# Performance work log

Hardware: AMD Instinct MI355X
Metric: run time of the kernel (lower is better)

## Reference

```python
import jax, jax.numpy as jnp
import numpy as np

NUM_HEADS = 16


def setup_inputs() -> dict:
    key = jax.random.key(0)
    ks = jax.random.split(key, 5)
    B, S, H = 2, 2048, 1024
    scale = 0.02
    return {
        "x": jax.random.normal(ks[0], (B, S, H), dtype=jnp.float32),
        "w_qkv": jax.random.normal(ks[1], (H, 3 * H), dtype=jnp.float32) * scale,
        "b_qkv": jax.random.normal(ks[2], (3 * H,), dtype=jnp.float32) * scale,
        "w_out": jax.random.normal(ks[3], (H, H), dtype=jnp.float32) * scale,
        "b_out": jax.random.normal(ks[4], (H,), dtype=jnp.float32) * scale,
    }


def reference(x, w_qkv, b_qkv, w_out, b_out):
    B, S, H = x.shape
    nh = NUM_HEADS
    hd = H // nh
    attn_scale = 1.0 / np.sqrt(hd).astype(np.float32)

    qkv = x @ w_qkv + b_qkv                       # (B, S, 3H)
    q, k, v = jnp.split(qkv, 3, axis=-1)
    # (B, S, H) -> (B, nh, S, hd)
    to_heads = lambda t: t.reshape(B, S, nh, hd).transpose(0, 2, 1, 3)
    q, k, v = to_heads(q), to_heads(k), to_heads(v)

    scores = jnp.einsum("bhid,bhjd->bhij", q, k) * attn_scale  # (B, nh, S, S)
    # Source masks where triu(ones)==0 -> strictly-lower triangle masked;
    # allowed positions are j >= i (attends to present and future).
    i = jnp.arange(S)[:, None]
    j = jnp.arange(S)[None, :]
    scores = jnp.where(j >= i, scores, -jnp.inf)
    attn = jax.nn.softmax(scores, axis=-1)        # dropout is identity (eval)

    out = jnp.einsum("bhij,bhjd->bhid", attn, v)  # (B, nh, S, hd)
    out = out.transpose(0, 2, 1, 3).reshape(B, S, H)
    return out @ w_out + b_out
```

## Files before the change

kernel.cpp:

```cpp
#include <hip/hip_runtime.h>
#include <hip/hip_bf16.h>
#include <stdint.h>
#include <stddef.h>

typedef __bf16 bf16_t;
typedef __bf16 bf16x4 __attribute__((ext_vector_type(4)));
typedef __bf16 bf16x8 __attribute__((ext_vector_type(8)));
typedef float f32x4 __attribute__((ext_vector_type(4)));

#define MFMA16(a, b, c) __builtin_amdgcn_mfma_f32_16x16x32_bf16(a, b, c, 0, 0, 0)

#define GLL16(g, l)                                                      \
    __builtin_amdgcn_global_load_lds(                                    \
        (const __attribute__((address_space(1))) void*)(g),              \
        (__attribute__((address_space(3))) void*)(l), 16, 0, 0)

#define SEQ 2048
#define NHEAD 16
#define HD 64
#define HID 1024
#define QKV_LD 3072
#define VT_LD 2080

__global__ void cast_f32_bf16(const float* __restrict__ in,
                              bf16_t* __restrict__ out, int n) {
    int i = (blockIdx.x * 256 + threadIdx.x) * 4;
    if (i < n) {
        float4 v = *(const float4*)(in + i);
        bf16x4 o = {(bf16_t)v.x, (bf16_t)v.y, (bf16_t)v.z, (bf16_t)v.w};
        *(bf16x4*)(out + i) = o;
    }
}

__global__ void transpose_cast(const float* __restrict__ W,
                               bf16_t* __restrict__ Wt, int K, int N) {
    __shared__ bf16_t tile[32][33];
    int n0 = blockIdx.x * 32, k0 = blockIdx.y * 32;
    int tx = threadIdx.x, ty = threadIdx.y;
#pragma unroll
    for (int i = 0; i < 4; i++)
        tile[ty + i * 8][tx] = (bf16_t)W[(size_t)(k0 + ty + i * 8) * N + n0 + tx];
    __syncthreads();
#pragma unroll
    for (int i = 0; i < 4; i++)
        Wt[(size_t)(n0 + ty + i * 8) * K + k0 + tx] = tile[tx][ty + i * 8];
}

__global__ __launch_bounds__(256)
void vt_transpose(const bf16_t* __restrict__ qkv, bf16_t* __restrict__ Vt) {
    int s0 = blockIdx.x * 64;
    int bh = blockIdx.y;
    int b = bh >> 4, h = bh & 15;
    int tid = threadIdx.x;
    __shared__ __align__(16) bf16_t tile[64][72];

    int row = tid >> 3, c8 = (tid & 7) * 8;
#pragma unroll
    for (int it = 0; it < 2; it++) {
        int sr = row + it * 32;
        bf16x8 v = *(const bf16x8*)(qkv + ((size_t)b * SEQ + s0 + sr) * QKV_LD +
                                    2 * HID + h * HD + c8);
        *(bf16x8*)(&tile[sr][c8]) = v;
    }
    __syncthreads();
#pragma unroll
    for (int it = 0; it < 2; it++) {
        int d = row + it * 32;
        bf16x8 w;
#pragma unroll
        for (int e = 0; e < 8; e++) w[e] = tile[c8 + e][d];
        *(bf16x8*)(Vt + ((size_t)bh * HD + d) * VT_LD + s0 + c8) = w;
    }
}

template <typename OutT>
__global__ __launch_bounds__(256)
void gemm_bt_bias(const bf16_t* __restrict__ A, const bf16_t* __restrict__ Bt,
                  const float* __restrict__ bias, OutT* __restrict__ C,
                  int M, int N, int K) {
    __shared__ __align__(16) bf16_t As[128][32];
    __shared__ __align__(16) bf16_t Bs[128][32];

    int m0 = blockIdx.y * 128;
    int n0 = blockIdx.x * 128;
    int tid = threadIdx.x;
    int wave = tid >> 6, lane = tid & 63;
    int quad = lane >> 4, l16 = lane & 15;
    int wm = (wave >> 1) * 64, wn = (wave & 1) * 64;

    f32x4 acc[4][4] = {};

    const bf16_t* a_base = A + (size_t)(m0 + wave * 32 + (lane >> 2)) * K + (lane & 3) * 8;
    const bf16_t* b_base = Bt + (size_t)(n0 + wave * 32 + (lane >> 2)) * K + (lane & 3) * 8;
    bf16_t* as_base = &As[wave * 32][0];
    bf16_t* bs_base = &Bs[wave * 32][0];

    for (int k0 = 0; k0 < K; k0 += 32) {
        GLL16(a_base + k0, as_base);
        GLL16(a_base + 16 * K + k0, as_base + 16 * 32);
        GLL16(b_base + k0, bs_base);
        GLL16(b_base + 16 * K + k0, bs_base + 16 * 32);
        __syncthreads();

        bf16x8 af[4], bfr[4];
#pragma unroll
        for (int t = 0; t < 4; t++)
            af[t] = *(const bf16x8*)(&As[wm + t * 16 + l16][quad * 8]);
#pragma unroll
        for (int t = 0; t < 4; t++)
            bfr[t] = *(const bf16x8*)(&Bs[wn + t * 16 + l16][quad * 8]);
#pragma unroll
        for (int mt = 0; mt < 4; mt++)
#pragma unroll
            for (int nt = 0; nt < 4; nt++)
                acc[mt][nt] = MFMA16(af[mt], bfr[nt], acc[mt][nt]);
        __syncthreads();
    }

#pragma unroll
    for (int mt = 0; mt < 4; mt++) {
        int row = m0 + wm + mt * 16 + quad * 4;
#pragma unroll
        for (int nt = 0; nt < 4; nt++) {
            int col = n0 + wn + nt * 16 + l16;
            float bv = bias[col];
#pragma unroll
            for (int r = 0; r < 4; r++)
                C[(size_t)(row + r) * N + col] = (OutT)(acc[mt][nt][r] + bv);
        }
    }
}

__global__ __launch_bounds__(256)
void attn_kernel(const bf16_t* __restrict__ qkv, const bf16_t* __restrict__ Vt,
                 bf16_t* __restrict__ attn_out) {
    int L = blockIdx.y * 16 + blockIdx.x;
    int xcd = L & 7, idx = L >> 3;
    int bh = xcd + 8 * (idx >> 4);
    int xb = idx & 15;
    int b = bh >> 4, h = bh & 15;

    int tid = threadIdx.x, wave = tid >> 6, lane = tid & 63;
    int quad = lane >> 4, l16 = lane & 15;

    const bf16_t* q_g = qkv + (size_t)b * SEQ * QKV_LD + (size_t)h * HD;
    const bf16_t* k_g = q_g + HID;
    const bf16_t* vt_g = Vt + (size_t)bh * HD * VT_LD;

    __shared__ __align__(16) bf16_t Ks[128][72];
    __shared__ __align__(16) bf16_t Vs[64][136];
    __shared__ __align__(16) bf16_t Ps[4][16][136];

    bf16x8 ones;
#pragma unroll
    for (int e = 0; e < 8; e++) ones[e] = (bf16_t)1.0f;

    int krow = tid >> 3, kc8 = (tid & 7) * 8;
    int vrow = tid >> 4, vc8 = (tid & 15) * 8;

#pragma unroll
    for (int phase = 0; phase < 2; phase++) {
        int tile = phase ? (31 - xb) : xb;
        int i0 = tile * 64;
        int iw = i0 + wave * 16;

        bf16x8 qa0 = *(const bf16x8*)(q_g + (size_t)(iw + l16) * QKV_LD + quad * 8);
        bf16x8 qa1 = *(const bf16x8*)(q_g + (size_t)(iw + l16) * QKV_LD + 32 + quad * 8);

        f32x4 o[4] = {};
        f32x4 lacc = {};

        for (int j0 = i0 & ~127; j0 < SEQ; j0 += 128) {
            __syncthreads();
#pragma unroll
            for (int t = 0; t < 4; t++) {
                bf16x8 kv = *(const bf16x8*)(k_g + (size_t)(j0 + krow + t * 32) * QKV_LD + kc8);
                *(bf16x8*)(&Ks[krow + t * 32][kc8]) = kv;
            }
#pragma unroll
            for (int t = 0; t < 4; t++) {
                bf16x8 vv = *(const bf16x8*)(vt_g + (size_t)(vrow + t * 16) * VT_LD + j0 + vc8);
                *(bf16x8*)(&Vs[vrow + t * 16][vc8]) = vv;
            }
            __syncthreads();

            f32x4 s[8];
#pragma unroll
            for (int jt = 0; jt < 8; jt++) {
                bf16x8 kb0 = *(const bf16x8*)(&Ks[jt * 16 + l16][quad * 8]);
                bf16x8 kb1 = *(const bf16x8*)(&Ks[jt * 16 + l16][32 + quad * 8]);
                f32x4 a = {};
                a = MFMA16(qa0, kb0, a);
                a = MFMA16(qa1, kb1, a);
                s[jt] = a;
            }

#pragma unroll
            for (int jt = 0; jt < 8; jt++) {
                int gj = j0 + jt * 16 + l16;
#pragma unroll
                for (int r = 0; r < 4; r++) {
                    int gi = iw + quad * 4 + r;
                    float p = (gj >= gi) ? __expf(s[jt][r] * 0.125f) : 0.0f;
                    Ps[wave][quad * 4 + r][jt * 16 + l16] = (bf16_t)p;
                }
            }

            bf16x8 pa[4];
#pragma unroll
            for (int kk = 0; kk < 4; kk++) {
                pa[kk] = *(const bf16x8*)(&Ps[wave][l16][kk * 32 + quad * 8]);
                lacc = MFMA16(pa[kk], ones, lacc);
            }

#pragma unroll
            for (int nt = 0; nt < 4; nt++) {
#pragma unroll
                for (int kk = 0; kk < 4; kk++) {
                    bf16x8 vb = *(const bf16x8*)(&Vs[nt * 16 + l16][kk * 32 + quad * 8]);
                    o[nt] = MFMA16(pa[kk], vb, o[nt]);
                }
            }
        }

#pragma unroll
        for (int r = 0; r < 4; r++) {
            int gi = iw + quad * 4 + r;
            float inv = 1.0f / lacc[r];
#pragma unroll
            for (int nt = 0; nt < 4; nt++)
                attn_out[(size_t)(b * SEQ + gi) * HID + h * HD + nt * 16 + l16] =
                    (bf16_t)(o[nt][r] * inv);
        }
    }
}

extern "C" void kernel_launch(void* const* d_in, const int* in_sizes, int n_in,
                              void* d_out, int out_size, void* d_ws, size_t ws_size,
                              hipStream_t stream) {
    const float* x     = (const float*)d_in[0];
    const float* w_qkv = (const float*)d_in[1];
    const float* b_qkv = (const float*)d_in[2];
    const float* w_out = (const float*)d_in[3];
    const float* b_out = (const float*)d_in[4];
    float* out = (float*)d_out;

    char* ws = (char*)d_ws;
    bf16_t* xbf   = (bf16_t*)(ws);
    bf16_t* Vt    = (bf16_t*)(ws);
    bf16_t* wqkvT = (bf16_t*)(ws + 8388608);
    bf16_t* woutT = (bf16_t*)(ws + 14680064);
    bf16_t* qkv   = (bf16_t*)(ws + 16777216);
    bf16_t* attn  = (bf16_t*)(ws + 41943040);

    cast_f32_bf16<<<4096, 256, 0, stream>>>(x, xbf, 4096 * 1024);

    transpose_cast<<<dim3(3072 / 32, 1024 / 32), dim3(32, 8), 0, stream>>>(
        w_qkv, wqkvT, 1024, 3072);
    transpose_cast<<<dim3(1024 / 32, 1024 / 32), dim3(32, 8), 0, stream>>>(
        w_out, woutT, 1024, 1024);

    gemm_bt_bias<bf16_t><<<dim3(3072 / 128, 4096 / 128), 256, 0, stream>>>(
        xbf, wqkvT, b_qkv, qkv, 4096, 3072, 1024);

    vt_transpose<<<dim3(SEQ / 64, 2 * NHEAD), 256, 0, stream>>>(qkv, Vt);

    attn_kernel<<<dim3(16, 2 * NHEAD), 256, 0, stream>>>(qkv, Vt, attn);

    gemm_bt_bias<float><<<dim3(1024 / 128, 4096 / 128), 256, 0, stream>>>(
        attn, woutT, b_out, out, 4096, 1024, 1024);
}
```

Before: 205.9 us.

## Fuse prep kernels, split attention tiles per block, narrow output GEMM tiles

Merges the x cast and both weight transpose-casts into one launch. The attention kernel now gives each block a single query tile instead of a paired short/long tile, which doubles the grid. It also reuses the K shared buffer for the P scratch (adding a barrier) and folds the softmax scale and log2e into Q so exp2 can be used. The causal mask is evaluated only on the first key block. The output projection GEMM uses 64-wide N tiles to put more blocks on the device, and attention gets a launch_bounds occupancy hint. The risks are load imbalance from unequal tile lengths, an extra barrier in each loop iteration, and extra bf16 rounding of the pre-scaled Q.

```diff
diff --git a/kernel.cpp b/kernel.cpp
--- a/kernel.cpp
+++ b/kernel.cpp
@@ -22,21 +22,33 @@
 #define QKV_LD 3072
 #define VT_LD 2080
 
-__global__ void cast_f32_bf16(const float* __restrict__ in,
-                              bf16_t* __restrict__ out, int n) {
-    int i = (blockIdx.x * 256 + threadIdx.x) * 4;
-    if (i < n) {
-        float4 v = *(const float4*)(in + i);
+__global__ __launch_bounds__(256)
+void prep_kernel(const float* __restrict__ x, const float* __restrict__ w_qkv,
+                 const float* __restrict__ w_out, bf16_t* __restrict__ xbf,
+                 bf16_t* __restrict__ wqkvT, bf16_t* __restrict__ woutT) {
+    int L = blockIdx.x;
+    int tid = threadIdx.x;
+    if (L < 4096) {
+        int i = (L * 256 + tid) * 4;
+        float4 v = *(const float4*)(x + i);
         bf16x4 o = {(bf16_t)v.x, (bf16_t)v.y, (bf16_t)v.z, (bf16_t)v.w};
-        *(bf16x4*)(out + i) = o;
-    }
-}
-
-__global__ void transpose_cast(const float* __restrict__ W,
-                               bf16_t* __restrict__ Wt, int K, int N) {
+        *(bf16x4*)(xbf + i) = o;
+        return;
+    }
     __shared__ bf16_t tile[32][33];
-    int n0 = blockIdx.x * 32, k0 = blockIdx.y * 32;
-    int tx = threadIdx.x, ty = threadIdx.y;
+    const float* W;
+    bf16_t* Wt;
+    int N, bx, by;
+    if (L < 7168) {
+        int r = L - 4096;
+        W = w_qkv; Wt = wqkvT; N = 3072; bx = r % 96; by = r / 96;
+    } else {
+        int r = L - 7168;
+        W = w_out; Wt = woutT; N = 1024; bx = r % 32; by = r / 32;
+    }
+    int K = 1024;
+    int n0 = bx * 32, k0 = by * 32;
+    int tx = tid & 31, ty = tid >> 5;
 #pragma unroll
     for (int i = 0; i < 4; i++)
         tile[ty + i * 8][tx] = (bf16_t)W[(size_t)(k0 + ty + i * 8) * N + n0 + tx];
@@ -73,46 +85,49 @@
     }
 }
 
-template <typename OutT>
+template <typename OutT, int TN>
 __global__ __launch_bounds__(256)
 void gemm_bt_bias(const bf16_t* __restrict__ A, const bf16_t* __restrict__ Bt,
                   const float* __restrict__ bias, OutT* __restrict__ C,
                   int M, int N, int K) {
+    constexpr int NT = TN / 32;
     __shared__ __align__(16) bf16_t As[128][32];
-    __shared__ __align__(16) bf16_t Bs[128][32];
+    __shared__ __align__(16) bf16_t Bs[TN][32];
 
     int m0 = blockIdx.y * 128;
-    int n0 = blockIdx.x * 128;
+    int n0 = blockIdx.x * TN;
     int tid = threadIdx.x;
     int wave = tid >> 6, lane = tid & 63;
     int quad = lane >> 4, l16 = lane & 15;
-    int wm = (wave >> 1) * 64, wn = (wave & 1) * 64;
-
-    f32x4 acc[4][4] = {};
-
-    const bf16_t* a_base = A + (size_t)(m0 + wave * 32 + (lane >> 2)) * K + (lane & 3) * 8;
-    const bf16_t* b_base = Bt + (size_t)(n0 + wave * 32 + (lane >> 2)) * K + (lane & 3) * 8;
+    int wm = (wave >> 1) * 64, wn = (wave & 1) * (TN / 2);
+
+    f32x4 acc[4][NT] = {};
+
+    const bf16_t* a_base =
+        A + (size_t)(m0 + wave * 32 + (lane >> 2)) * K + (lane & 3) * 8;
+    const bf16_t* b_base =
+        Bt + (size_t)(n0 + wave * (TN / 4) + (lane >> 2)) * K + (lane & 3) * 8;
     bf16_t* as_base = &As[wave * 32][0];
-    bf16_t* bs_base = &Bs[wave * 32][0];
+    bf16_t* bs_base = &Bs[wave * (TN / 4)][0];
 
     for (int k0 = 0; k0 < K; k0 += 32) {
         GLL16(a_base + k0, as_base);
         GLL16(a_base + 16 * K + k0, as_base + 16 * 32);
         GLL16(b_base + k0, bs_base);
-        GLL16(b_base + 16 * K + k0, bs_base + 16 * 32);
-        __syncthreads();
-
-        bf16x8 af[4], bfr[4];
+        if (TN == 128) GLL16(b_base + 16 * K + k0, bs_base + 16 * 32);
+        __syncthreads();
+
+        bf16x8 af[4], bfr[NT];
 #pragma unroll
         for (int t = 0; t < 4; t++)
             af[t] = *(const bf16x8*)(&As[wm + t * 16 + l16][quad * 8]);
 #pragma unroll
-        for (int t = 0; t < 4; t++)
+        for (int t = 0; t < NT; t++)
             bfr[t] = *(const bf16x8*)(&Bs[wn + t * 16 + l16][quad * 8]);
 #pragma unroll
         for (int mt = 0; mt < 4; mt++)
 #pragma unroll
-            for (int nt = 0; nt < 4; nt++)
+            for (int nt = 0; nt < NT; nt++)
                 acc[mt][nt] = MFMA16(af[mt], bfr[nt], acc[mt][nt]);
         __syncthreads();
     }
@@ -121,7 +136,7 @@
     for (int mt = 0; mt < 4; mt++) {
         int row = m0 + wm + mt * 16 + quad * 4;
 #pragma unroll
-        for (int nt = 0; nt < 4; nt++) {
+        for (int nt = 0; nt < NT; nt++) {
             int col = n0 + wn + nt * 16 + l16;
             float bv = bias[col];
 #pragma unroll
@@ -131,13 +146,13 @@
     }
 }
 
-__global__ __launch_bounds__(256)
+__global__ __launch_bounds__(256, 4)
 void attn_kernel(const bf16_t* __restrict__ qkv, const bf16_t* __restrict__ Vt,
                  bf16_t* __restrict__ attn_out) {
-    int L = blockIdx.y * 16 + blockIdx.x;
-    int xcd = L & 7, idx = L >> 3;
-    int bh = xcd + 8 * (idx >> 4);
-    int xb = idx & 15;
+    int L = blockIdx.y * 32 + blockIdx.x;
+    int xcd = L & 7, s5 = L >> 3;
+    int bh = xcd + 8 * (s5 >> 5);
+    int tile = s5 & 31;
     int b = bh >> 4, h = bh & 15;
 
     int tid = threadIdx.x, wave = tid >> 6, lane = tid & 63;
@@ -149,89 +164,106 @@
 
     __shared__ __align__(16) bf16_t Ks[128][72];
     __shared__ __align__(16) bf16_t Vs[64][136];
-    __shared__ __align__(16) bf16_t Ps[4][16][136];
+    bf16_t* Ps_w = &Ks[wave * 32][0];
 
     bf16x8 ones;
 #pragma unroll
     for (int e = 0; e < 8; e++) ones[e] = (bf16_t)1.0f;
+
+    int i0 = tile * 64;
+    int iw = i0 + wave * 16;
+
+    const float QS = 0.125f * 1.44269504088896f;
+    bf16x8 qa0, qa1;
+    {
+        bf16x8 t0 = *(const bf16x8*)(q_g + (size_t)(iw + l16) * QKV_LD + quad * 8);
+        bf16x8 t1 = *(const bf16x8*)(q_g + (size_t)(iw + l16) * QKV_LD + 32 + quad * 8);
+#pragma unroll
+        for (int e = 0; e < 8; e++) {
+            qa0[e] = (bf16_t)((float)t0[e] * QS);
+            qa1[e] = (bf16_t)((float)t1[e] * QS);
+        }
+    }
+
+    f32x4 o[4] = {};
+    f32x4 lacc = {};
 
     int krow = tid >> 3, kc8 = (tid & 7) * 8;
     int vrow = tid >> 4, vc8 = (tid & 15) * 8;
 
-#pragma unroll
-    for (int phase = 0; phase < 2; phase++) {
-        int tile = phase ? (31 - xb) : xb;
-        int i0 = tile * 64;
-        int iw = i0 + wave * 16;
-
-        bf16x8 qa0 = *(const bf16x8*)(q_g + (size_t)(iw + l16) * QKV_LD + quad * 8);
-        bf16x8 qa1 = *(const bf16x8*)(q_g + (size_t)(iw + l16) * QKV_LD + 32 + quad * 8);
-
-        f32x4 o[4] = {};
-        f32x4 lacc = {};
-
-        for (int j0 = i0 & ~127; j0 < SEQ; j0 += 128) {
-            __syncthreads();
-#pragma unroll
-            for (int t = 0; t < 4; t++) {
-                bf16x8 kv = *(const bf16x8*)(k_g + (size_t)(j0 + krow + t * 32) * QKV_LD + kc8);
-                *(bf16x8*)(&Ks[krow + t * 32][kc8]) = kv;
-            }
-#pragma unroll
-            for (int t = 0; t < 4; t++) {
-                bf16x8 vv = *(const bf16x8*)(vt_g + (size_t)(vrow + t * 16) * VT_LD + j0 + vc8);
-                *(bf16x8*)(&Vs[vrow + t * 16][vc8]) = vv;
-            }
-            __syncthreads();
-
-            f32x4 s[8];
-#pragma unroll
-            for (int jt = 0; jt < 8; jt++) {
-                bf16x8 kb0 = *(const bf16x8*)(&Ks[jt * 16 + l16][quad * 8]);
-                bf16x8 kb1 = *(const bf16x8*)(&Ks[jt * 16 + l16][32 + quad * 8]);
-                f32x4 a = {};
-                a = MFMA16(qa0, kb0, a);
-                a = MFMA16(qa1, kb1, a);
-                s[jt] = a;
-            }
-
+    int jstart = i0 & ~127;
+    for (int j0 = jstart; j0 < SEQ; j0 += 128) {
+        __syncthreads();
+#pragma unroll
+        for (int t = 0; t < 4; t++) {
+            bf16x8 kv = *(const bf16x8*)(k_g + (size_t)(j0 + krow + t * 32) * QKV_LD + kc8);
+            *(bf16x8*)(&Ks[krow + t * 32][kc8]) = kv;
+        }
+#pragma unroll
+        for (int t = 0; t < 4; t++) {
+            bf16x8 vv = *(const bf16x8*)(vt_g + (size_t)(vrow + t * 16) * VT_LD + j0 + vc8);
+            *(bf16x8*)(&Vs[vrow + t * 16][vc8]) = vv;
+        }
+        __syncthreads();
+
+        f32x4 s[8];
+#pragma unroll
+        for (int jt = 0; jt < 8; jt++) {
+            bf16x8 kb0 = *(const bf16x8*)(&Ks[jt * 16 + l16][quad * 8]);
+            bf16x8 kb1 = *(const bf16x8*)(&Ks[jt * 16 + l16][32 + quad * 8]);
+            f32x4 a = {};
+            a = MFMA16(qa0, kb0, a);
+            a = MFMA16(qa1, kb1, a);
+            s[jt] = a;
+        }
+
+        __syncthreads();
+
+        if (j0 == jstart) {
 #pragma unroll
             for (int jt = 0; jt < 8; jt++) {
                 int gj = j0 + jt * 16 + l16;
 #pragma unroll
                 for (int r = 0; r < 4; r++) {
                     int gi = iw + quad * 4 + r;
-                    float p = (gj >= gi) ? __expf(s[jt][r] * 0.125f) : 0.0f;
-                    Ps[wave][quad * 4 + r][jt * 16 + l16] = (bf16_t)p;
+                    float p = (gj >= gi) ? __builtin_amdgcn_exp2f(s[jt][r]) : 0.0f;
+                    Ps_w[(quad * 4 + r) * 136 + jt * 16 + l16] = (bf16_t)p;
                 }
             }
-
-            bf16x8 pa[4];
+        } else {
+#pragma unroll
+            for (int jt = 0; jt < 8; jt++)
+#pragma unroll
+                for (int r = 0; r < 4; r++)
+                    Ps_w[(quad * 4 + r) * 136 + jt * 16 + l16] =
+                        (bf16_t)__builtin_amdgcn_exp2f(s[jt][r]);
+        }
+
+        bf16x8 pa[4];
+#pragma unroll
+        for (int kk = 0; kk < 4; kk++) {
+            pa[kk] = *(const bf16x8*)(&Ps_w[l16 * 136 + kk * 32 + quad * 8]);
+            lacc = MFMA16(pa[kk], ones, lacc);
+        }
+
+#pragma unroll
+        for (int nt = 0; nt < 4; nt++) {
 #pragma unroll
             for (int kk = 0; kk < 4; kk++) {
-                pa[kk] = *(const bf16x8*)(&Ps[wave][l16][kk * 32 + quad * 8]);
-                lacc = MFMA16(pa[kk], ones, lacc);
+                bf16x8 vb = *(const bf16x8*)(&Vs[nt * 16 + l16][kk * 32 + quad * 8]);
+                o[nt] = MFMA16(pa[kk], vb, o[nt]);
             }
-
-#pragma unroll
-            for (int nt = 0; nt < 4; nt++) {
-#pragma unroll
-                for (int kk = 0; kk < 4; kk++) {
-                    bf16x8 vb = *(const bf16x8*)(&Vs[nt * 16 + l16][kk * 32 + quad * 8]);
-                    o[nt] = MFMA16(pa[kk], vb, o[nt]);
-                }
-            }
-        }
-
-#pragma unroll
-        for (int r = 0; r < 4; r++) {
-            int gi = iw + quad * 4 + r;
-            float inv = 1.0f / lacc[r];
-#pragma unroll
-            for (int nt = 0; nt < 4; nt++)
-                attn_out[(size_t)(b * SEQ + gi) * HID + h * HD + nt * 16 + l16] =
-                    (bf16_t)(o[nt][r] * inv);
-        }
+        }
+    }
+
+#pragma unroll
+    for (int r = 0; r < 4; r++) {
+        int gi = iw + quad * 4 + r;
+        float inv = 1.0f / lacc[r];
+#pragma unroll
+        for (int nt = 0; nt < 4; nt++)
+            attn_out[(size_t)(b * SEQ + gi) * HID + h * HD + nt * 16 + l16] =
+                (bf16_t)(o[nt][r] * inv);
     }
 }
 
@@ -253,20 +285,15 @@
     bf16_t* qkv   = (bf16_t*)(ws + 16777216);
     bf16_t* attn  = (bf16_t*)(ws + 41943040);
 
-    cast_f32_bf16<<<4096, 256, 0, stream>>>(x, xbf, 4096 * 1024);
-
-    transpose_cast<<<dim3(3072 / 32, 1024 / 32), dim3(32, 8), 0, stream>>>(
-        w_qkv, wqkvT, 1024, 3072);
-    transpose_cast<<<dim3(1024 / 32, 1024 / 32), dim3(32, 8), 0, stream>>>(
-        w_out, woutT, 1024, 1024);
-
-    gemm_bt_bias<bf16_t><<<dim3(3072 / 128, 4096 / 128), 256, 0, stream>>>(
+    prep_kernel<<<8192, 256, 0, stream>>>(x, w_qkv, w_out, xbf, wqkvT, woutT);
+
+    gemm_bt_bias<bf16_t, 128><<<dim3(3072 / 128, 4096 / 128), 256, 0, stream>>>(
         xbf, wqkvT, b_qkv, qkv, 4096, 3072, 1024);
 
     vt_transpose<<<dim3(SEQ / 64, 2 * NHEAD), 256, 0, stream>>>(qkv, Vt);
 
-    attn_kernel<<<dim3(16, 2 * NHEAD), 256, 0, stream>>>(qkv, Vt, attn);
-
-    gemm_bt_bias<float><<<dim3(1024 / 128, 4096 / 128), 256, 0, stream>>>(
+    attn_kernel<<<dim3(32, 2 * NHEAD), 256, 0, stream>>>(qkv, Vt, attn);
+
+    gemm_bt_bias<float, 64><<<dim3(1024 / 64, 4096 / 128), 256, 0, stream>>>(
         attn, woutT, b_out, out, 4096, 1024, 1024);
 }
```

Result: slower. 216.3 us (+5.0%).
